# Kernel optimization log

Hardware: AMD Instinct MI355X
Metric: run time of the kernel (lower is better)

Reference implementation:

```python
import jax, jax.numpy as jnp
import numpy as np

B, S, D, H = 2, 2048, 1024, 16
DK = D // H
NEG = -1.0e9


def setup_inputs() -> dict:
    key = jax.random.key(0)
    ks = jax.random.split(key, 12)
    scale = 1.0 / np.sqrt(D)
    return {
        "Q": jax.random.normal(ks[0], (B, S, D), jnp.float32),
        "K": jax.random.normal(ks[1], (B, S, D), jnp.float32),
        "V": jax.random.normal(ks[2], (B, S, D), jnp.float32),
        "Wq": jax.random.normal(ks[3], (D, D), jnp.float32) * scale,
        "bq": jnp.zeros((D,), jnp.float32),
        "Wk": jax.random.normal(ks[4], (D, D), jnp.float32) * scale,
        "bk": jnp.zeros((D,), jnp.float32),
        "Wv": jax.random.normal(ks[5], (D, D), jnp.float32) * scale,
        "bv": jnp.zeros((D,), jnp.float32),
        "Wo": jax.random.normal(ks[6], (D, D), jnp.float32) * scale,
        "bo": jnp.zeros((D,), jnp.float32),
        "src_mask": jnp.ones((B, S), jnp.int32),
    }


def reference(Q, K, V, Wq, bq, Wk, bk, Wv, bv, Wo, bo, src_mask):
    # Dropout layers are identity in eval mode.
    def heads(x, W, b):
        y = x @ W + b                      # [B,S,D]
        return y.reshape(B, S, H, DK).transpose(0, 2, 1, 3)  # [B,H,S,DK]

    q = heads(Q, Wq, bq)
    k = heads(K, Wk, bk)
    v = heads(V, Wv, bv)

    scores = jnp.einsum("bhqd,bhkd->bhqk", q, k) / np.sqrt(DK)  # [B,H,S,S]
    mask = src_mask[:, None, None, :]  # [B,1,1,S] broadcasts over heads/queries
    scores = jnp.where(mask == 0, NEG, scores)
    attn = jax.nn.softmax(scores, axis=-1)
    out = jnp.einsum("bhqk,bhkd->bhqd", attn, v)  # [B,H,S,DK]
    out = out.transpose(0, 2, 1, 3).reshape(B, S, D)
    return out @ Wo + bo
```

## Files before the change

kernel.cpp:

```cpp
#include <hip/hip_runtime.h>
#include <hip/hip_bf16.h>
#include <cstdint>

#define B_ 2
#define S_ 2048
#define D_ 1024
#define H_ 16
#define DK_ 64

typedef __bf16 bf16x8 __attribute__((ext_vector_type(8)));
typedef float f32x4 __attribute__((ext_vector_type(4)));
typedef unsigned int u32x4 __attribute__((ext_vector_type(4)));

typedef __attribute__((address_space(3))) void lds_void_t;
typedef const __attribute__((address_space(1))) void gbl_void_t;

__device__ __forceinline__ unsigned short f2bf(float x) {
    unsigned int u = __builtin_bit_cast(unsigned int, x);
    u += 0x7fffu + ((u >> 16) & 1u);
    return (unsigned short)(u >> 16);
}

__device__ __forceinline__ float exp2fast(float x) {
    float r;
    asm("v_exp_f32 %0, %1" : "=v"(r) : "v"(x));
    return r;
}

__device__ __forceinline__ unsigned cvtpk(float a, float b) {
    unsigned r;
    asm("v_cvt_pk_bf16_f32 %0, %1, %2" : "=v"(r) : "v"(a), "v"(b));
    return r;
}

__device__ __forceinline__ void gload16(const void* g, void* lds) {
    __builtin_amdgcn_global_load_lds((gbl_void_t*)(uintptr_t)g,
                                     (lds_void_t*)(unsigned)(uintptr_t)lds,
                                     16, 0, 0);
}

__device__ __forceinline__ bf16x8 lds_read8(const unsigned short* p) {
    return __builtin_bit_cast(bf16x8, *(const u32x4*)p);
}

__device__ __forceinline__ f32x4 mfma16(bf16x8 a, bf16x8 b, f32x4 c) {
    return __builtin_amdgcn_mfma_f32_16x16x32_bf16(a, b, c, 0, 0, 0);
}

__global__ void prep_w_kernel(const float* __restrict__ Wq, const float* __restrict__ Wk,
                              const float* __restrict__ Wv, const float* __restrict__ Wo,
                              unsigned short* __restrict__ WqT, unsigned short* __restrict__ WkT,
                              unsigned short* __restrict__ WvT, unsigned short* __restrict__ WoT) {
    const int wsel = blockIdx.x >> 10;
    const int rem  = blockIdx.x & 1023;
    const int bx = rem & 31, by = rem >> 5;
    const float* W = (wsel == 0) ? Wq : (wsel == 1) ? Wk : (wsel == 2) ? Wv : Wo;
    unsigned short* Wt = (wsel == 0) ? WqT : (wsel == 1) ? WkT : (wsel == 2) ? WvT : WoT;
    __shared__ float t[32][33];
    const int tx = threadIdx.x & 31, ty = threadIdx.x >> 5;
#pragma unroll
    for (int j = 0; j < 4; j++)
        t[ty + 8 * j][tx] = W[(size_t)(by * 32 + ty + 8 * j) * D_ + bx * 32 + tx];
    __syncthreads();
#pragma unroll
    for (int j = 0; j < 4; j++)
        Wt[(size_t)(bx * 32 + ty + 8 * j) * D_ + by * 32 + tx] = f2bf(t[tx][ty + 8 * j]);
}

__global__ __launch_bounds__(256, 3) void qkv_gemm(
    const float* __restrict__ Qf, const float* __restrict__ Kf,
    const float* __restrict__ Vf, const unsigned short* __restrict__ WqT,
    const unsigned short* __restrict__ WkT, const unsigned short* __restrict__ WvT,
    const float* __restrict__ bq, const float* __restrict__ bk,
    const float* __restrict__ bvv, unsigned short* __restrict__ qb,
    unsigned short* __restrict__ kb, unsigned short* __restrict__ vTb, float qs) {
    constexpr int Kd = 1024;
    __shared__ __align__(16) unsigned short As[128 * 32];
    __shared__ __align__(16) unsigned short Bs[128 * 32];
    __shared__ __align__(16) unsigned short Cs[128 * 136];
    const int z = blockIdx.z;
    const float* Af = (z == 0) ? Qf : (z == 1) ? Kf : Vf;
    const unsigned short* Bt = (z == 0) ? WqT : (z == 1) ? WkT : WvT;
    const float* bias = (z == 0) ? bq : (z == 1) ? bk : bvv;
    const float cscale = (z == 0) ? qs : 1.0f;

    const int tid = threadIdx.x;
    const int l = tid & 63, w = tid >> 6;
    const int lr = l & 15, g = l >> 4;
    const int wr = w & 1, wc = w >> 1;

    const int wg  = blockIdx.x + 8 * blockIdx.y;
    const int eff = (wg & 7) * 32 + (wg >> 3);
    const int n0  = (eff & 7) * 128;
    const int m0  = (eff >> 3) * 128;

    f32x4 acc[4][4] = {};

    const int arow = tid >> 3;
    const int acol = (tid & 3) * 8 + ((tid >> 2) & 1) * 4;
    const float* a_base = Af + (size_t)(m0 + arow) * Kd + acol;

    const int mr = tid >> 2;
    const int kk = (tid & 3) * 8;
    const unsigned short* b_src = Bt + (size_t)(n0 + mr) * Kd + kk;
    char* bsb = (char*)Bs + w * 1024;

    float4 areg[4];
#pragma unroll
    for (int i = 0; i < 4; i++)
        areg[i] = *reinterpret_cast<const float4*>(a_base + (size_t)(32 * i) * Kd);

    for (int k0 = 0; k0 < Kd; k0 += 32) {
        __syncthreads();
        gload16(b_src + k0,           bsb);
        gload16(b_src + 64 * Kd + k0, bsb + 4096);
#pragma unroll
        for (int i = 0; i < 4; i++) {
            uint2 pk;
            pk.x = cvtpk(areg[i].x, areg[i].y);
            pk.y = cvtpk(areg[i].z, areg[i].w);
            *reinterpret_cast<uint2*>(&As[(arow + 32 * i) * 32 + acol]) = pk;
        }
        __syncthreads();
        if (k0 + 32 < Kd) {
#pragma unroll
            for (int i = 0; i < 4; i++)
                areg[i] = *reinterpret_cast<const float4*>(
                    a_base + (size_t)(32 * i) * Kd + k0 + 32);
        }
        bf16x8 av[4], bv[4];
#pragma unroll
        for (int mi = 0; mi < 4; mi++)
            av[mi] = lds_read8(&As[(wr * 64 + mi * 16 + lr) * 32 + g * 8]);
#pragma unroll
        for (int ni = 0; ni < 4; ni++)
            bv[ni] = lds_read8(&Bs[(wc * 64 + ni * 16 + lr) * 32 + g * 8]);
#pragma unroll
        for (int mi = 0; mi < 4; mi++)
#pragma unroll
            for (int ni = 0; ni < 4; ni++)
                acc[mi][ni] = mfma16(av[mi], bv[ni], acc[mi][ni]);
    }

    if (z == 2) {
#pragma unroll
        for (int ni = 0; ni < 4; ni++) {
            const int cl = wc * 64 + ni * 16 + lr;
            const float bcol = bias[n0 + cl];
#pragma unroll
            for (int mi = 0; mi < 4; mi++) {
                const int rw = wr * 64 + mi * 16 + 4 * g;
                uint2 pk;
                pk.x = cvtpk(acc[mi][ni][0] + bcol, acc[mi][ni][1] + bcol);
                pk.y = cvtpk(acc[mi][ni][2] + bcol, acc[mi][ni][3] + bcol);
                *reinterpret_cast<uint2*>(&Cs[cl * 136 + rw]) = pk;
            }
        }
        __syncthreads();
        const int s0g = m0 & 2047;
        const int bb  = m0 >> 11;
#pragma unroll
        for (int it = 0; it < 8; ++it) {
            const int cl = it * 16 + (tid >> 4);
            const int sc = tid & 15;
            const int cg = n0 + cl;
            const int hh = cg >> 6, dk = cg & 63;
            const u32x4 vv = *reinterpret_cast<const u32x4*>(&Cs[cl * 136 + sc * 8]);
            *reinterpret_cast<u32x4*>(
                &vTb[(((size_t)(bb * H_ + hh) * DK_ + dk) << 11) + s0g + sc * 8]) = vv;
        }
    } else {
#pragma unroll
        for (int ni = 0; ni < 4; ni++) {
            const int col = n0 + wc * 64 + ni * 16 + lr;
            const float bcol = bias[col];
#pragma unroll
            for (int mi = 0; mi < 4; mi++) {
#pragma unroll
                for (int r = 0; r < 4; r++) {
                    const int row = m0 + wr * 64 + mi * 16 + 4 * g + r;
                    const float v = (acc[mi][ni][r] + bcol) * cscale;
                    const int b = row >> 11, s = row & 2047, h = col >> 6, dk = col & 63;
                    unsigned short* out = z ? kb : qb;
                    out[(((size_t)(b * H_ + h) * S_ + s) << 6) + dk] = f2bf(v);
                }
            }
        }
    }
}

__global__ __launch_bounds__(256, 3) void gemm_out(
    const unsigned short* __restrict__ A, const unsigned short* __restrict__ Bt,
    const float* __restrict__ bias, float* __restrict__ C) {
    constexpr int Kd = 1024;
    __shared__ __align__(16) unsigned short As[128 * 32];
    __shared__ __align__(16) unsigned short Bs[128 * 32];
    const int tid = threadIdx.x;
    const int l = tid & 63, w = tid >> 6;
    const int lr = l & 15, g = l >> 4;
    const int wr = w & 1, wc = w >> 1;

    const int wg  = blockIdx.x + 8 * blockIdx.y;
    const int eff = (wg & 7) * 32 + (wg >> 3);
    const int n0  = (eff & 7) * 128;
    const int m0  = (eff >> 3) * 128;

    f32x4 acc[4][4] = {};
    const int mr = tid >> 2;
    const int kk = (tid & 3) * 8;
    const unsigned short* a_src = A + (size_t)(m0 + mr) * Kd + kk;
    const unsigned short* b_src = Bt + (size_t)(n0 + mr) * Kd + kk;
    char* asb = (char*)As + w * 1024;
    char* bsb = (char*)Bs + w * 1024;

    for (int k0 = 0; k0 < Kd; k0 += 32) {
        __syncthreads();
        gload16(a_src + k0,           asb);
        gload16(a_src + 64 * Kd + k0, asb + 4096);
        gload16(b_src + k0,           bsb);
        gload16(b_src + 64 * Kd + k0, bsb + 4096);
        __syncthreads();
        bf16x8 av[4], bv[4];
#pragma unroll
        for (int mi = 0; mi < 4; mi++)
            av[mi] = lds_read8(&As[(wr * 64 + mi * 16 + lr) * 32 + g * 8]);
#pragma unroll
        for (int ni = 0; ni < 4; ni++)
            bv[ni] = lds_read8(&Bs[(wc * 64 + ni * 16 + lr) * 32 + g * 8]);
#pragma unroll
        for (int mi = 0; mi < 4; mi++)
#pragma unroll
            for (int ni = 0; ni < 4; ni++)
                acc[mi][ni] = mfma16(av[mi], bv[ni], acc[mi][ni]);
    }

#pragma unroll
    for (int ni = 0; ni < 4; ni++) {
        const int col = n0 + wc * 64 + ni * 16 + lr;
        const float bcol = bias[col];
#pragma unroll
        for (int mi = 0; mi < 4; mi++)
#pragma unroll
            for (int r = 0; r < 4; r++) {
                const int row = m0 + wr * 64 + mi * 16 + 4 * g + r;
                C[(size_t)row * D_ + col] = acc[mi][ni][r] + bcol;
            }
    }
}

__global__ __launch_bounds__(512, 4) void attn64(
    const unsigned short* __restrict__ q, const unsigned short* __restrict__ kmat,
    const unsigned short* __restrict__ vT, const int* __restrict__ mask,
    unsigned short* __restrict__ aout) {
    __shared__ __align__(16) unsigned short k_lds[2][64 * 64];
    __shared__ __align__(16) unsigned short v_lds[2][64 * 64];
    __shared__ __align__(16) unsigned short p_lds[8][16 * 72];
    __shared__ int mflag;

    const int tid = threadIdx.x;
    const int l = tid & 63, w = tid >> 6;
    const int lr = l & 15, g = l >> 4;

    const int wg  = blockIdx.x + 16 * blockIdx.y;
    const int eff = (wg & 7) * 64 + (wg >> 3);
    const int q0  = (eff & 15) * 128;
    const int bh  = eff >> 4;
    const int b = bh >> 4, h = bh & 15;

    const size_t base = (size_t)bh * S_ * DK_;
    const size_t vbase = (size_t)bh * DK_ * S_;
    const float FM = 14.0f;

    bf16x8 qf[2];
#pragma unroll
    for (int ks = 0; ks < 2; ks++)
        qf[ks] = __builtin_bit_cast(bf16x8,
            *(const u32x4*)(q + base + (size_t)(q0 + w * 16 + lr) * 64 + ks * 32 + g * 8));

    const u32x4 ones_u = {0x3F803F80u, 0x3F803F80u, 0x3F803F80u, 0x3F803F80u};
    const bf16x8 ones = __builtin_bit_cast(bf16x8, ones_u);

    f32x4 O[4] = {};
    f32x4 lrun = {};
    unsigned short* pw = &p_lds[w][0];

    const int srow = tid >> 3;
    const int ssl  = (tid & 7) ^ (srow & 7);
    const unsigned short* ksrc = kmat + base + (size_t)srow * DK_ + ssl * 8;
    const unsigned short* vsrc = vT + vbase + (size_t)srow * S_ + ssl * 8;
    const int* mrow = mask + b * S_;

    if (tid == 0) mflag = 0;
    gload16(ksrc, (char*)&k_lds[0][0] + w * 1024);
    gload16(vsrc, (char*)&v_lds[0][0] + w * 1024);
    int ok = 1;
#pragma unroll
    for (int i = 0; i < 4; i++) ok &= (mrow[tid + i * 512] != 0);
    __syncthreads();
    if (!__all(ok)) mflag = 1;
    __syncthreads();
    const int maskany = mflag;

    auto body = [&](int t, const unsigned short* kc, const unsigned short* vc,
                    char* kn, char* vn, bool pf) {
        const int kv0 = t * 64;
        if (pf) {
            gload16(ksrc + (size_t)(kv0 + 64) * DK_, kn + w * 1024);
            gload16(vsrc + (kv0 + 64),               vn + w * 1024);
        }

        f32x4 sacc[4];
        __builtin_amdgcn_s_setprio(1);
#pragma unroll
        for (int n = 0; n < 4; n++) {
            const int row = n * 16 + lr;
            const int x = lr & 7;
            bf16x8 kf0 = lds_read8(&kc[row * 64 + (g ^ x) * 8]);
            bf16x8 kf1 = lds_read8(&kc[row * 64 + ((4 + g) ^ x) * 8]);
            f32x4 s = {};
            s = mfma16(kf0, qf[0], s);
            s = mfma16(kf1, qf[1], s);
            sacc[n] = s;
        }
        __builtin_amdgcn_s_setprio(0);

        if (maskany) {
#pragma unroll
            for (int n = 0; n < 4; n++) {
                const int4 mm = *reinterpret_cast<const int4*>(&mrow[kv0 + n * 16 + 4 * g]);
                sacc[n][0] = mm.x ? sacc[n][0] : -3.0e8f;
                sacc[n][1] = mm.y ? sacc[n][1] : -3.0e8f;
                sacc[n][2] = mm.z ? sacc[n][2] : -3.0e8f;
                sacc[n][3] = mm.w ? sacc[n][3] : -3.0e8f;
            }
        }

#pragma unroll
        for (int n = 0; n < 4; n++) {
            const float e0 = exp2fast(sacc[n][0] - FM);
            const float e1 = exp2fast(sacc[n][1] - FM);
            const float e2 = exp2fast(sacc[n][2] - FM);
            const float e3 = exp2fast(sacc[n][3] - FM);
            uint2 pk;
            pk.x = cvtpk(e0, e1);
            pk.y = cvtpk(e2, e3);
            *reinterpret_cast<uint2*>(&pw[lr * 72 + n * 16 + 4 * g]) = pk;
        }

        f32x4 osum = {};
        __builtin_amdgcn_s_setprio(1);
#pragma unroll
        for (int k2 = 0; k2 < 2; k2++) {
            bf16x8 pa = lds_read8(&pw[lr * 72 + k2 * 32 + 8 * g]);
            osum = mfma16(pa, ones, osum);
#pragma unroll
            for (int n = 0; n < 4; n++) {
                const int row = n * 16 + lr;
                const int ph = (k2 * 4 + g) ^ (lr & 7);
                bf16x8 bvf = lds_read8(&vc[row * 64 + ph * 8]);
                O[n] = mfma16(pa, bvf, O[n]);
            }
        }
        __builtin_amdgcn_s_setprio(0);
        lrun += osum;

        __syncthreads();
    };

    for (int t = 0; t < S_ / 64; t += 2) {
        body(t,     &k_lds[0][0], &v_lds[0][0], (char*)&k_lds[1][0], (char*)&v_lds[1][0],
             true);
        body(t + 1, &k_lds[1][0], &v_lds[1][0], (char*)&k_lds[0][0], (char*)&v_lds[0][0],
             t + 2 < S_ / 64);
    }

#pragma unroll
    for (int r = 0; r < 4; r++) {
        const float inv = 1.0f / lrun[r];
        const int srw = q0 + w * 16 + 4 * g + r;
#pragma unroll
        for (int n = 0; n < 4; n++) {
            const int col = h * 64 + n * 16 + lr;
            aout[(size_t)(b * S_ + srw) * D_ + col] = f2bf(O[n][r] * inv);
        }
    }
}

extern "C" void kernel_launch(void* const* d_in, const int* in_sizes, int n_in,
                              void* d_out, int out_size, void* d_ws, size_t ws_size,
                              hipStream_t stream) {
    const float* Q  = (const float*)d_in[0];
    const float* K  = (const float*)d_in[1];
    const float* V  = (const float*)d_in[2];
    const float* Wq = (const float*)d_in[3];
    const float* bq = (const float*)d_in[4];
    const float* Wk = (const float*)d_in[5];
    const float* bk = (const float*)d_in[6];
    const float* Wv = (const float*)d_in[7];
    const float* bv = (const float*)d_in[8];
    const float* Wo = (const float*)d_in[9];
    const float* bo = (const float*)d_in[10];
    const int*   mk = (const int*)d_in[11];

    char* ws = (char*)d_ws;
    unsigned short* WqT = (unsigned short*)(ws + (24ull << 20));
    unsigned short* WkT = (unsigned short*)(ws + (26ull << 20));
    unsigned short* WvT = (unsigned short*)(ws + (28ull << 20));
    unsigned short* WoT = (unsigned short*)(ws + (30ull << 20));
    unsigned short* qb  = (unsigned short*)(ws + (32ull << 20));
    unsigned short* kb  = (unsigned short*)(ws + (40ull << 20));
    unsigned short* vTb = (unsigned short*)(ws + (48ull << 20));
    unsigned short* ab  = (unsigned short*)(ws + (56ull << 20));

    prep_w_kernel<<<4096, 256, 0, stream>>>(Wq, Wk, Wv, Wo, WqT, WkT, WvT, WoT);

    const float qs = 0.125f * 1.44269504088896340736f;
    dim3 gq(8, 32, 3);
    qkv_gemm<<<gq, 256, 0, stream>>>(Q, K, V, WqT, WkT, WvT,
                                     bq, bk, bv, qb, kb, vTb, qs);

    dim3 ag(16, 32);
    attn64<<<ag, 512, 0, stream>>>(qb, kb, vTb, mk, ab);

    dim3 gg(8, 32);
    gemm_out<<<gg, 256, 0, stream>>>(ab, WoT, bo, (float*)d_out);
}
```

Before: 113.5 us.

## Double QKV GEMM k-tile to 64, swizzle B LDS layout, alias C staging buffer

Result: slower. 123.1 us (+8.5%).

```diff
diff --git a/kernel.cpp b/kernel.cpp
--- a/kernel.cpp
+++ b/kernel.cpp
@@ -67,7 +67,7 @@
         Wt[(size_t)(bx * 32 + ty + 8 * j) * D_ + by * 32 + tx] = f2bf(t[tx][ty + 8 * j]);
 }
 
-__global__ __launch_bounds__(256, 3) void qkv_gemm(
+__global__ __launch_bounds__(256, 4) void qkv_gemm(
     const float* __restrict__ Qf, const float* __restrict__ Kf,
     const float* __restrict__ Vf, const unsigned short* __restrict__ WqT,
     const unsigned short* __restrict__ WkT, const unsigned short* __restrict__ WvT,
@@ -75,9 +75,11 @@
     const float* __restrict__ bvv, unsigned short* __restrict__ qb,
     unsigned short* __restrict__ kb, unsigned short* __restrict__ vTb, float qs) {
     constexpr int Kd = 1024;
-    __shared__ __align__(16) unsigned short As[128 * 32];
-    __shared__ __align__(16) unsigned short Bs[128 * 32];
-    __shared__ __align__(16) unsigned short Cs[128 * 136];
+    __shared__ __align__(16) char smem[34816];
+    unsigned short* As = (unsigned short*)smem;
+    unsigned short* Bs = (unsigned short*)(smem + 18432);
+    unsigned short* Cs = (unsigned short*)smem;
+
     const int z = blockIdx.z;
     const float* Af = (z == 0) ? Qf : (z == 1) ? Kf : Vf;
     const unsigned short* Bt = (z == 0) ? WqT : (z == 1) ? WkT : WvT;
@@ -97,50 +99,66 @@
     f32x4 acc[4][4] = {};
 
     const int arow = tid >> 3;
-    const int acol = (tid & 3) * 8 + ((tid >> 2) & 1) * 4;
-    const float* a_base = Af + (size_t)(m0 + arow) * Kd + acol;
-
-    const int mr = tid >> 2;
-    const int kk = (tid & 3) * 8;
-    const unsigned short* b_src = Bt + (size_t)(n0 + mr) * Kd + kk;
-    char* bsb = (char*)Bs + w * 1024;
-
-    float4 areg[4];
+    const int ac   = (tid & 7) * 8;
+    const float* a_base = Af + (size_t)(m0 + arow) * Kd + ac;
+    const int brow  = tid >> 3;
+    const int bslot = (tid & 7) ^ (brow & 7);
+    const unsigned short* b_src = Bt + (size_t)(n0 + brow) * Kd + bslot * 8;
+
+    float4 areg[4][2];
 #pragma unroll
     for (int i = 0; i < 4; i++)
-        areg[i] = *reinterpret_cast<const float4*>(a_base + (size_t)(32 * i) * Kd);
-
-    for (int k0 = 0; k0 < Kd; k0 += 32) {
-        __syncthreads();
-        gload16(b_src + k0,           bsb);
-        gload16(b_src + 64 * Kd + k0, bsb + 4096);
+#pragma unroll
+        for (int j = 0; j < 2; j++)
+            areg[i][j] = *reinterpret_cast<const float4*>(
+                a_base + (size_t)(32 * i) * Kd + 4 * j);
+
+    for (int k0 = 0; k0 < Kd; k0 += 64) {
+        __syncthreads();
+#pragma unroll
+        for (int s = 0; s < 4; s++)
+            gload16(b_src + (size_t)(s * 32) * Kd + k0,
+                    (char*)Bs + s * 4096 + tid * 16);
 #pragma unroll
         for (int i = 0; i < 4; i++) {
-            uint2 pk;
-            pk.x = cvtpk(areg[i].x, areg[i].y);
-            pk.y = cvtpk(areg[i].z, areg[i].w);
-            *reinterpret_cast<uint2*>(&As[(arow + 32 * i) * 32 + acol]) = pk;
-        }
-        __syncthreads();
-        if (k0 + 32 < Kd) {
+            const int row = arow + 32 * i;
+            uint2 p0, p1;
+            p0.x = cvtpk(areg[i][0].x, areg[i][0].y);
+            p0.y = cvtpk(areg[i][0].z, areg[i][0].w);
+            p1.x = cvtpk(areg[i][1].x, areg[i][1].y);
+            p1.y = cvtpk(areg[i][1].z, areg[i][1].w);
+            *reinterpret_cast<uint2*>(&As[row * 72 + ac]) = p0;
+            *reinterpret_cast<uint2*>(&As[row * 72 + ac + 4]) = p1;
+        }
+        __syncthreads();
+        if (k0 + 64 < Kd) {
 #pragma unroll
             for (int i = 0; i < 4; i++)
-                areg[i] = *reinterpret_cast<const float4*>(
-                    a_base + (size_t)(32 * i) * Kd + k0 + 32);
-        }
-        bf16x8 av[4], bv[4];
-#pragma unroll
-        for (int mi = 0; mi < 4; mi++)
-            av[mi] = lds_read8(&As[(wr * 64 + mi * 16 + lr) * 32 + g * 8]);
-#pragma unroll
-        for (int ni = 0; ni < 4; ni++)
-            bv[ni] = lds_read8(&Bs[(wc * 64 + ni * 16 + lr) * 32 + g * 8]);
-#pragma unroll
-        for (int mi = 0; mi < 4; mi++)
-#pragma unroll
-            for (int ni = 0; ni < 4; ni++)
-                acc[mi][ni] = mfma16(av[mi], bv[ni], acc[mi][ni]);
-    }
+#pragma unroll
+                for (int j = 0; j < 2; j++)
+                    areg[i][j] = *reinterpret_cast<const float4*>(
+                        a_base + (size_t)(32 * i) * Kd + k0 + 64 + 4 * j);
+        }
+#pragma unroll
+        for (int ks = 0; ks < 2; ks++) {
+            bf16x8 av[4], bv[4];
+#pragma unroll
+            for (int mi = 0; mi < 4; mi++)
+                av[mi] = lds_read8(&As[(wr * 64 + mi * 16 + lr) * 72 + ks * 32 + g * 8]);
+#pragma unroll
+            for (int ni = 0; ni < 4; ni++) {
+                const int row = wc * 64 + ni * 16 + lr;
+                const int ph = (ks * 4 + g) ^ (lr & 7);
+                bv[ni] = lds_read8(&Bs[row * 64 + ph * 8]);
+            }
+#pragma unroll
+            for (int mi = 0; mi < 4; mi++)
+#pragma unroll
+                for (int ni = 0; ni < 4; ni++)
+                    acc[mi][ni] = mfma16(av[mi], bv[ni], acc[mi][ni]);
+        }
+    }
+    __syncthreads();
 
     if (z == 2) {
 #pragma unroll
```
